# Optimization experiments

Measured on AMD Instinct MI355X. Metric: run time of the kernel, lower is better.

Reference implementation:

```python
import jax, jax.numpy as jnp
import numpy as np

B, C, H, W = 16, 64, 128, 128
C8 = C // 8

def setup_inputs() -> dict:
    key = jax.random.key(0)
    ks = jax.random.split(key, 9)
    s = 0.05
    return {
        "x": jax.random.normal(ks[0], (B, C, H, W), jnp.float32),
        "y": jax.random.normal(ks[1], (B, C, H, W), jnp.float32),
        "query_w": jax.random.normal(ks[2], (C8, C), jnp.float32) * s,
        "query_b": jax.random.normal(ks[3], (C8,), jnp.float32) * s,
        "key_w": jax.random.normal(ks[4], (C8, C), jnp.float32) * s,
        "key_b": jax.random.normal(ks[5], (C8,), jnp.float32) * s,
        "value_w": jax.random.normal(ks[6], (C, 2 * C), jnp.float32) * s,
        "value_b": jax.random.normal(ks[7], (C,), jnp.float32) * s,
        "gamma": jax.random.normal(ks[8], (), jnp.float32) * 0.1,
    }

def _conv1x1(t, w, b):
    # t: [B, Cin, H, W], w: [Cout, Cin] -> [B, Cout, H, W]
    return jnp.einsum('oc,bchw->bohw', w, t) + b[None, :, None, None]

def reference(x, y, query_w, query_b, key_w, key_b, value_w, value_b, gamma):
    b, c, h, w = x.shape
    q = _conv1x1(x, query_w, query_b)                       # [B, C8, H, W]
    k = _conv1x1(y, key_w, key_b)                           # [B, C8, H, W]
    v = _conv1x1(jnp.concatenate([x, y], axis=1), value_w, value_b)  # [B, C, H, W]

    # axial energies: H-axis (g indexes key rows), W-axis (u indexes key cols)
    energy_H = jnp.einsum('bchw,bcgw->bhwg', q, k)          # [B, H, W, H]
    energy_W = jnp.einsum('bchw,bchu->bhwu', q, k)          # [B, H, W, W]

    # -inf on the H diagonal (self position counted once, via the W branch)
    eye = jnp.eye(h, dtype=bool)                            # [H, H]
    energy_H = jnp.where(eye[None, :, None, :], -jnp.inf, energy_H)

    att = jax.nn.softmax(jnp.concatenate([energy_H, energy_W], axis=3), axis=3)
    att_H = att[..., :h]                                    # [B, H, W, H]
    att_W = att[..., h:]                                    # [B, H, W, W]

    out_H = jnp.einsum('bcgw,bhwg->bchw', v, att_H)
    out_W = jnp.einsum('bchu,bhwu->bchw', v, att_W)
    return gamma * (out_H + out_W) + x + y
```

## Files before the change

kernel.cpp:

```cpp
#include <hip/hip_runtime.h>

#define NCH 80
#define HW 16384

typedef unsigned short u16;
typedef unsigned int u32;
typedef short s16x8 __attribute__((ext_vector_type(8)));
typedef float f32x4 __attribute__((ext_vector_type(4)));

__device__ __forceinline__ float b2f_lo(u32 pk){ union{u32 u; float f;} c; c.u = pk<<16; return c.f; }
__device__ __forceinline__ float b2f_hi(u32 pk){ union{u32 u; float f;} c; c.u = pk & 0xffff0000u; return c.f; }
__device__ __forceinline__ float b2f(u16 v){ union{u32 u; float f;} c; c.u = ((u32)v)<<16; return c.f; }
__device__ __forceinline__ u16 f2b_hw(float f){
    union{ __bf16 h; u16 s; } c; c.h = (__bf16)f; return c.s;
}
__device__ __forceinline__ u32 pk2(float a, float b){
    return (u32)f2b_hw(a) | ((u32)f2b_hw(b)<<16);
}
#define NEG_INF (-__builtin_inff())

__global__ __launch_bounds__(256) void k_wcvt(
    const float* __restrict__ qw, const float* __restrict__ qb,
    const float* __restrict__ kw, const float* __restrict__ kb,
    const float* __restrict__ vw, const float* __restrict__ vb,
    u16* __restrict__ wbf, float* __restrict__ bias80)
{
    int i = blockIdx.x*256 + threadIdx.x;
    int ch = i >> 7, cin = i & 127;
    float v;
    if (ch < 8)       v = (cin < 64) ? qw[ch*64 + cin] : 0.f;
    else if (ch < 16) v = (cin >= 64) ? kw[(ch-8)*64 + (cin-64)] : 0.f;
    else              v = vw[(ch-16)*128 + cin];
    wbf[i] = f2b_hw(v);
    if (i < 80){
        bias80[i] = (i<8) ? qb[i] : (i<16) ? kb[i-8] : vb[i-16];
    }
}

__global__ __launch_bounds__(256) void k_qkv_mfma(
    const float* __restrict__ x, const float* __restrict__ y,
    const u16* __restrict__ wbf, const float* __restrict__ bias80,
    u16* __restrict__ qkv, u16* __restrict__ xy)
{
    int t = threadIdx.x;
    int wv = t >> 6, l = t & 63;
    int lm = l & 15, q = l >> 4;
    int p0 = blockIdx.x * 64 + wv * 16;
    int b = p0 >> 14, rem = p0 & 16383;

    const float* xb = x + (size_t)b*64*HW + rem + lm;
    const float* yb = y + (size_t)b*64*HW + rem + lm;
    float xf[4][8];
    #pragma unroll
    for (int ks=0; ks<4; ks++){
        const float* srcp = (ks < 2) ? xb : yb;
        int cin0 = (ks & 1)*32 + q*8;
        #pragma unroll
        for (int j=0;j<8;j++) xf[ks][j] = srcp[(size_t)(cin0 + j)*HW];
    }
    s16x8 af[4];
    #pragma unroll
    for (int ks=0; ks<4; ks++)
        #pragma unroll
        for (int j=0;j<8;j++) af[ks][j] = (short)f2b_hw(xf[ks][j]);

    if (xy){
        #pragma unroll
        for (int half=0; half<2; half++)
            #pragma unroll
            for (int j=0;j<8;j++){
                int c = half*32 + q*8 + j;
                xy[(size_t)(b*64+c)*HW + rem + lm] = f2b_hw(xf[half][j] + xf[half+2][j]);
            }
    }

    f32x4 acc[5];
    #pragma unroll
    for (int mt=0; mt<5; mt++) acc[mt] = (f32x4){0.f,0.f,0.f,0.f};

    #pragma unroll
    for (int mt=0; mt<5; mt++){
        int ch = mt*16 + lm;
        const u16* wrow = wbf + ch*128 + q*8;
        #pragma unroll
        for (int ks=0; ks<4; ks++){
            s16x8 bfrag = *(const s16x8*)(wrow + ks*32);
            acc[mt] = __builtin_amdgcn_mfma_f32_16x16x32_bf16(af[ks], bfrag, acc[mt], 0, 0, 0);
        }
    }

    #pragma unroll
    for (int mt=0; mt<5; mt++){
        int ch = mt*16 + lm;
        float bs = bias80[ch];
        u32 lo = pk2(acc[mt][0]+bs, acc[mt][1]+bs);
        u32 hi = pk2(acc[mt][2]+bs, acc[mt][3]+bs);
        *(uint2*)&qkv[(size_t)(b*NCH + ch)*HW + rem + q*4] = make_uint2(lo, hi);
    }
}

__global__ __launch_bounds__(256) void k_tr(const u16* __restrict__ src, u16* __restrict__ dst)
{
    __shared__ u16 tile[64][65];
    int blk = blockIdx.x;
    int plane = blk >> 2, tq = blk & 3;
    int r0 = (tq >> 1) * 64, c0 = (tq & 1) * 64;
    const u16* s = src + (size_t)plane * HW;
    u16* d = dst + (size_t)plane * HW;
    int col = threadIdx.x & 63, rr = threadIdx.x >> 6;
    #pragma unroll
    for (int k=0;k<16;k++){
        int r = k*4 + rr;
        tile[r][col] = s[(r0+r)*128 + c0 + col];
    }
    __syncthreads();
    #pragma unroll
    for (int k=0;k<16;k++){
        int r = k*4 + rr;
        d[(c0+r)*128 + r0 + col] = tile[col][r];
    }
}

__global__ __launch_bounds__(512, 4) void k_col(
    const u16* __restrict__ qkvT, u16* __restrict__ colT,
    float* __restrict__ mH, float* __restrict__ sH)
{
    __shared__ __align__(16) float q_s[8*128];
    __shared__ __align__(16) float k_sw[8*128];
    __shared__ __align__(16) u16  v_bf[64*128];
    __shared__ __align__(16) u16  p_bf[128*128];

    int t = threadIdx.x;
    int b = blockIdx.x >> 7, w = blockIdx.x & 127;
    const u32* src = (const u32*)(qkvT + (size_t)b*NCH*HW + w*128);
    u32* v32 = (u32*)v_bf;
    u32* p32 = (u32*)p_bf;

    #pragma unroll
    for (int r=0;r<2;r++){
        int idx = t + r*512;
        int ch = idx >> 6, hp = idx & 63;
        u32 pk = src[ch*8192 + hp];
        int g0 = hp*2;
        if (ch < 8){
            *(float2*)&q_s[ch*128 + g0] = make_float2(b2f_lo(pk), b2f_hi(pk));
        } else {
            int o = ch - 8;
            k_sw[g0*8     + (o ^ ((g0>>3)&7))]     = b2f_lo(pk);
            k_sw[(g0+1)*8 + (o ^ (((g0+1)>>3)&7))] = b2f_hi(pk);
        }
    }
    #pragma unroll
    for (int r=0;r<8;r++){
        int idx = t + r*512;
        int c = idx >> 6, gp = idx & 63;
        v32[(c*64 + gp) ^ ((c&7)<<2)] = src[(16+c)*8192 + gp];
    }
    __syncthreads();

    int tr = t >> 4, tc = t & 15;
    int h0 = tr*4, g0 = tc*8;
    float e[4][8];
    #pragma unroll
    for (int i=0;i<4;i++)
        #pragma unroll
        for (int j=0;j<8;j++) e[i][j] = 0.f;

    #pragma unroll
    for (int o=0;o<8;o++){
        float qv[4], kv[8];
        #pragma unroll
        for (int i=0;i<4;i++) qv[i] = q_s[o*128 + h0 + i];
        int kb = o ^ (tc & 7);
        #pragma unroll
        for (int j=0;j<8;j++) kv[j] = k_sw[(g0+j)*8 + kb];
        #pragma unroll
        for (int i=0;i<4;i++)
            #pragma unroll
            for (int j=0;j<8;j++) e[i][j] += qv[i]*kv[j];
    }
    #pragma unroll
    for (int i=0;i<4;i++){
        int h = h0 + i;
        if ((h>>3) == tc) e[i][h&7] = NEG_INF;
    }
    #pragma unroll
    for (int i=0;i<4;i++){
        int h = h0 + i;
        float m = e[i][0];
        #pragma unroll
        for (int j=1;j<8;j++) m = fmaxf(m, e[i][j]);
        m = fmaxf(m, __shfl_xor(m,1));
        m = fmaxf(m, __shfl_xor(m,2));
        m = fmaxf(m, __shfl_xor(m,4));
        m = fmaxf(m, __shfl_xor(m,8));
        float s = 0.f;
        #pragma unroll
        for (int j=0;j<8;j++){ float pp = __expf(e[i][j]-m); e[i][j]=pp; s += pp; }
        s += __shfl_xor(s,1);
        s += __shfl_xor(s,2);
        s += __shfl_xor(s,4);
        s += __shfl_xor(s,8);
        if (tc == 0){
            mH[b*HW + h*128 + w] = m;
            sH[b*HW + h*128 + w] = s;
        }
        uint4 pw;
        pw.x = pk2(e[i][0], e[i][1]);
        pw.y = pk2(e[i][2], e[i][3]);
        pw.z = pk2(e[i][4], e[i][5]);
        pw.w = pk2(e[i][6], e[i][7]);
        *(uint4*)&p32[(h*64 + tc*4) ^ ((h&7)<<2)] = pw;
    }
    __syncthreads();

    int wv = t >> 6, l = t & 63;
    int lm = l & 15, lq = l >> 4;
    int mt = wv;
    f32x4 acc[4];
    #pragma unroll
    for (int nt=0; nt<4; nt++) acc[nt] = (f32x4){0.f,0.f,0.f,0.f};

    #pragma unroll
    for (int ks=0; ks<4; ks++){
        int ri = mt*16 + lm;
        s16x8 a = *(const s16x8*)&p32[(ri*64 + ks*16 + lq*4) ^ ((ri&7)<<2)];
        #pragma unroll
        for (int nt=0; nt<4; nt++){
            int c = nt*16 + lm;
            s16x8 bf_ = *(const s16x8*)&v32[(c*64 + ks*16 + lq*4) ^ ((c&7)<<2)];
            acc[nt] = __builtin_amdgcn_mfma_f32_16x16x32_bf16(a, bf_, acc[nt], 0, 0, 0);
        }
    }
    #pragma unroll
    for (int nt=0; nt<4; nt++){
        int c = nt*16 + lm;
        int hh = mt*16 + lq*4;
        uint2 st;
        st.x = pk2(acc[nt][0], acc[nt][1]);
        st.y = pk2(acc[nt][2], acc[nt][3]);
        *(uint2*)&colT[((size_t)(b*64+c)*128 + w)*128 + hh] = st;
    }
}

__global__ __launch_bounds__(512, 4) void k_row(
    const u16* __restrict__ qkv, const u16* __restrict__ colpart,
    const float* __restrict__ mH, const float* __restrict__ sH,
    const float* __restrict__ x, const float* __restrict__ y,
    const u16* __restrict__ xy,
    const float* __restrict__ gamma_p, float* __restrict__ out)
{
    __shared__ __align__(16) float q_s[8*128];
    __shared__ __align__(16) float k_sw[8*128];
    __shared__ __align__(16) u16  v_bf[64*128];
    __shared__ __align__(16) u16  p_bf[128*128];
    __shared__ float fc_s[128], fr_s[128];

    int t = threadIdx.x;
    int b = blockIdx.x >> 7, h = blockIdx.x & 127;
    const u32* src = (const u32*)(qkv + (size_t)b*NCH*HW + h*128);
    u32* v32 = (u32*)v_bf;
    u32* p32 = (u32*)p_bf;

    #pragma unroll
    for (int r=0;r<2;r++){
        int idx = t + r*512;
        int ch = idx >> 6, wp = idx & 63;
        u32 pk = src[ch*8192 + wp];
        int u0 = wp*2;
        if (ch < 8){
            *(float2*)&q_s[ch*128 + u0] = make_float2(b2f_lo(pk), b2f_hi(pk));
        } else {
            int o = ch - 8;
            k_sw[u0*8     + (o ^ ((u0>>3)&7))]     = b2f_lo(pk);
            k_sw[(u0+1)*8 + (o ^ (((u0+1)>>3)&7))] = b2f_hi(pk);
        }
    }
    #pragma unroll
    for (int r=0;r<8;r++){
        int idx = t + r*512;
        int c = idx >> 6, up = idx & 63;
        v32[(c*64 + up) ^ ((c&7)<<2)] = src[(16+c)*8192 + up];
    }
    __syncthreads();

    int tr = t >> 4, tc = t & 15;
    int w0 = tr*4, u0 = tc*8;
    float e[4][8];
    #pragma unroll
    for (int i=0;i<4;i++)
        #pragma unroll
        for (int j=0;j<8;j++) e[i][j] = 0.f;

    #pragma unroll
    for (int o=0;o<8;o++){
        float qv[4], kv[8];
        #pragma unroll
        for (int i=0;i<4;i++) qv[i] = q_s[o*128 + w0 + i];
        int kb = o ^ (tc & 7);
        #pragma unroll
        for (int j=0;j<8;j++) kv[j] = k_sw[(u0+j)*8 + kb];
        #pragma unroll
        for (int i=0;i<4;i++)
            #pragma unroll
            for (int j=0;j<8;j++) e[i][j] += qv[i]*kv[j];
    }
    int pixbase = b*HW + h*128;
    #pragma unroll
    for (int i=0;i<4;i++){
        int wp = w0 + i;
        float m = e[i][0];
        #pragma unroll
        for (int j=1;j<8;j++) m = fmaxf(m, e[i][j]);
        m = fmaxf(m, __shfl_xor(m,1));
        m = fmaxf(m, __shfl_xor(m,2));
        m = fmaxf(m, __shfl_xor(m,4));
        m = fmaxf(m, __shfl_xor(m,8));
        float mh = mH[pixbase + wp];
        float sh = sH[pixbase + wp];
        float mg = fmaxf(m, mh);
        float s = 0.f;
        #pragma unroll
        for (int j=0;j<8;j++){ float pp = __expf(e[i][j]-mg); e[i][j]=pp; s += pp; }
        s += __shfl_xor(s,1);
        s += __shfl_xor(s,2);
        s += __shfl_xor(s,4);
        s += __shfl_xor(s,8);
        if (tc == 0){
            float ef = __expf(mh - mg);
            float stot = sh*ef + s;
            fc_s[wp] = ef/stot;
            fr_s[wp] = 1.0f/stot;
        }
        uint4 pw;
        pw.x = pk2(e[i][0], e[i][1]);
        pw.y = pk2(e[i][2], e[i][3]);
        pw.z = pk2(e[i][4], e[i][5]);
        pw.w = pk2(e[i][6], e[i][7]);
        *(uint4*)&p32[(wp*64 + tc*4) ^ ((wp&7)<<2)] = pw;
    }
    __syncthreads();

    int wv = t >> 6, l = t & 63;
    int lm = l & 15, lq = l >> 4;
    int mt = wv;
    f32x4 acc[4];
    #pragma unroll
    for (int nt=0; nt<4; nt++) acc[nt] = (f32x4){0.f,0.f,0.f,0.f};

    #pragma unroll
    for (int ks=0; ks<4; ks++){
        int ri = mt*16 + lm;
        s16x8 a = *(const s16x8*)&p32[(ri*64 + ks*16 + lq*4) ^ ((ri&7)<<2)];
        #pragma unroll
        for (int nt=0; nt<4; nt++){
            int c = nt*16 + lm;
            s16x8 bf_ = *(const s16x8*)&v32[(c*64 + ks*16 + lq*4) ^ ((c&7)<<2)];
            acc[nt] = __builtin_amdgcn_mfma_f32_16x16x32_bf16(a, bf_, acc[nt], 0, 0, 0);
        }
    }
    float gm = gamma_p[0];
    int wq0 = mt*16 + lq*4;
    float fcv[4], frv[4];
    #pragma unroll
    for (int r2=0;r2<4;r2++){ fcv[r2] = fc_s[wq0+r2]; frv[r2] = fr_s[wq0+r2]; }

    #pragma unroll
    for (int nt=0; nt<4; nt++){
        int c = nt*16 + lm;
        size_t off = ((size_t)(b*64+c)*128 + h)*128 + wq0;
        uint2 cpv = *(const uint2*)&colpart[off];
        float cp[4] = {b2f_lo(cpv.x), b2f_hi(cpv.x), b2f_lo(cpv.y), b2f_hi(cpv.y)};
        float xs[4];
        if (xy){
            uint2 xv = *(const uint2*)&xy[off];
            xs[0]=b2f_lo(xv.x); xs[1]=b2f_hi(xv.x); xs[2]=b2f_lo(xv.y); xs[3]=b2f_hi(xv.y);
        } else {
            float4 x4 = *(const float4*)&x[off];
            float4 y4 = *(const float4*)&y[off];
            xs[0]=x4.x+y4.x; xs[1]=x4.y+y4.y; xs[2]=x4.z+y4.z; xs[3]=x4.w+y4.w;
        }
        float4 o4;
        o4.x = gm*(cp[0]*fcv[0] + acc[nt][0]*frv[0]) + xs[0];
        o4.y = gm*(cp[1]*fcv[1] + acc[nt][1]*frv[1]) + xs[1];
        o4.z = gm*(cp[2]*fcv[2] + acc[nt][2]*frv[2]) + xs[2];
        o4.w = gm*(cp[3]*fcv[3] + acc[nt][3]*frv[3]) + xs[3];
        *(float4*)&out[off] = o4;
    }
}

extern "C" void kernel_launch(void* const* d_in, const int* in_sizes, int n_in,
                              void* d_out, int out_size, void* d_ws, size_t ws_size,
                              hipStream_t stream)
{
    (void)in_sizes; (void)n_in; (void)out_size;
    const float* x  = (const float*)d_in[0];
    const float* y  = (const float*)d_in[1];
    const float* qw = (const float*)d_in[2];
    const float* qb = (const float*)d_in[3];
    const float* kw = (const float*)d_in[4];
    const float* kb = (const float*)d_in[5];
    const float* vw = (const float*)d_in[6];
    const float* vb = (const float*)d_in[7];
    const float* gm = (const float*)d_in[8];
    float* out = (float*)d_out;

    char* ws = (char*)d_ws;
    u16* qkv     = (u16*)(ws);
    u16* qkvT    = (u16*)(ws + 41943040ull);
    u16* colT    = (u16*)(ws + 83886080ull);
    u16* colpart = qkvT;
    float* mH    = (float*)(ws + 117440512ull);
    float* sH    = (float*)(ws + 118489088ull);
    u16* wbf     = (u16*)(ws + 119537664ull);
    float* bias80= (float*)(ws + 119558144ull);
    u16* xybuf   = nullptr;
    if (ws_size >= 119603200ull + 33554432ull)
        xybuf = (u16*)(ws + 119603200ull);

    k_wcvt<<<40, 256, 0, stream>>>(qw, qb, kw, kb, vw, vb, wbf, bias80);
    k_qkv_mfma<<<4096, 256, 0, stream>>>(x, y, wbf, bias80, qkv, xybuf);
    k_tr <<<5120, 256, 0, stream>>>(qkv, qkvT);
    k_col<<<2048, 512, 0, stream>>>(qkvT, colT, mH, sH);
    k_tr <<<4096, 256, 0, stream>>>(colT, colpart);
    k_row<<<2048, 512, 0, stream>>>(qkv, colpart, mH, sH, x, y, xybuf, gm, out);
}
```

Before: 193.5 us.

## Stage QKV projection inputs through LDS with vectorized loads and packed xy writes

The QKV projection kernel now loads x/y with float4 reads into a padded shared-memory tile of bf16 pairs, then builds MFMA A-fragments from LDS. Each block covers 128 pixels instead of 64, so the grid is halved. The xy sum buffer is written as packed u32 pairs instead of scalar u16 stores. This targets the uncoalesced scalar global loads and narrow stores of the old version, at the cost of about 33 KB of LDS per block and a block-wide barrier. The xy sum is now computed from bf16-rounded inputs rather than the fp32 values, which changes numerics slightly.

Result: faster. 180.7 us (-6.6%).

```diff
diff --git a/kernel.cpp b/kernel.cpp
--- a/kernel.cpp
+++ b/kernel.cpp
@@ -18,6 +18,8 @@
     return (u32)f2b_hw(a) | ((u32)f2b_hw(b)<<16);
 }
 #define NEG_INF (-__builtin_inff())
+
+union U4S8 { uint4 u; s16x8 v; };
 
 __global__ __launch_bounds__(256) void k_wcvt(
     const float* __restrict__ qw, const float* __restrict__ qb,
@@ -37,65 +39,83 @@
     }
 }
 
-__global__ __launch_bounds__(256) void k_qkv_mfma(
+__global__ __launch_bounds__(256, 4) void k_qkv_mfma(
     const float* __restrict__ x, const float* __restrict__ y,
     const u16* __restrict__ wbf, const float* __restrict__ bias80,
     u16* __restrict__ qkv, u16* __restrict__ xy)
 {
+    __shared__ u32 a32[128*65];
+
     int t = threadIdx.x;
+    int p0 = blockIdx.x * 128;
+    int b = p0 >> 14, rem = p0 & 16383;
+    const float* xb = x + (size_t)b*64*HW + rem;
+    const float* yb = y + (size_t)b*64*HW + rem;
+
+    #pragma unroll
+    for (int r=0;r<8;r++){
+        int idx = t + r*256;
+        int cp = idx >> 5;
+        int pxg = (idx & 31) * 4;
+        const float* srcp = (cp < 32) ? xb : yb;
+        int c0 = (cp & 31)*2;
+        float4 fa = *(const float4*)&srcp[(size_t)c0*HW + pxg];
+        float4 fb = *(const float4*)&srcp[(size_t)(c0+1)*HW + pxg];
+        a32[(pxg+0)*65 + cp] = pk2(fa.x, fb.x);
+        a32[(pxg+1)*65 + cp] = pk2(fa.y, fb.y);
+        a32[(pxg+2)*65 + cp] = pk2(fa.z, fb.z);
+        a32[(pxg+3)*65 + cp] = pk2(fa.w, fb.w);
+    }
+    __syncthreads();
+
+    if (xy){
+        #pragma unroll
+        for (int r=0;r<16;r++){
+            int idx = t + r*256;
+            int c = idx >> 6;
+            int pxp = idx & 63;
+            int cpx = c >> 1, cpy = 32 + (c >> 1);
+            u32 wx0 = a32[(2*pxp)*65 + cpx], wx1 = a32[(2*pxp+1)*65 + cpx];
+            u32 wy0 = a32[(2*pxp)*65 + cpy], wy1 = a32[(2*pxp+1)*65 + cpy];
+            float xv0 = (c&1)? b2f_hi(wx0) : b2f_lo(wx0);
+            float xv1 = (c&1)? b2f_hi(wx1) : b2f_lo(wx1);
+            float yv0 = (c&1)? b2f_hi(wy0) : b2f_lo(wy0);
+            float yv1 = (c&1)? b2f_hi(wy1) : b2f_lo(wy1);
+            size_t xw = ((size_t)(b*64+c)*HW + rem) >> 1;
+            ((u32*)xy)[xw + pxp] = pk2(xv0+yv0, xv1+yv1);
+        }
+    }
+
     int wv = t >> 6, l = t & 63;
-    int lm = l & 15, q = l >> 4;
-    int p0 = blockIdx.x * 64 + wv * 16;
-    int b = p0 >> 14, rem = p0 & 16383;
-
-    const float* xb = x + (size_t)b*64*HW + rem + lm;
-    const float* yb = y + (size_t)b*64*HW + rem + lm;
-    float xf[4][8];
-    #pragma unroll
-    for (int ks=0; ks<4; ks++){
-        const float* srcp = (ks < 2) ? xb : yb;
-        int cin0 = (ks & 1)*32 + q*8;
-        #pragma unroll
-        for (int j=0;j<8;j++) xf[ks][j] = srcp[(size_t)(cin0 + j)*HW];
-    }
-    s16x8 af[4];
-    #pragma unroll
-    for (int ks=0; ks<4; ks++)
-        #pragma unroll
-        for (int j=0;j<8;j++) af[ks][j] = (short)f2b_hw(xf[ks][j]);
-
-    if (xy){
-        #pragma unroll
-        for (int half=0; half<2; half++)
+    int lm = l & 15, lq = l >> 4;
+
+    #pragma unroll
+    for (int m2=0;m2<2;m2++){
+        int pxl = (wv*2 + m2)*16 + lm;
+        s16x8 af[4];
+        #pragma unroll
+        for (int ks=0;ks<4;ks++){
+            int wbase = pxl*65 + ks*16 + lq*4;
+            U4S8 uu;
+            uu.u = make_uint4(a32[wbase], a32[wbase+1], a32[wbase+2], a32[wbase+3]);
+            af[ks] = uu.v;
+        }
+        #pragma unroll
+        for (int nt=0;nt<5;nt++){
+            int ch = nt*16 + lm;
+            const u16* wrow = wbf + ch*128 + lq*8;
+            f32x4 acc = (f32x4){0.f,0.f,0.f,0.f};
             #pragma unroll
-            for (int j=0;j<8;j++){
-                int c = half*32 + q*8 + j;
-                xy[(size_t)(b*64+c)*HW + rem + lm] = f2b_hw(xf[half][j] + xf[half+2][j]);
+            for (int ks=0;ks<4;ks++){
+                s16x8 bfrag = *(const s16x8*)(wrow + ks*32);
+                acc = __builtin_amdgcn_mfma_f32_16x16x32_bf16(af[ks], bfrag, acc, 0, 0, 0);
             }
-    }
-
-    f32x4 acc[5];
-    #pragma unroll
-    for (int mt=0; mt<5; mt++) acc[mt] = (f32x4){0.f,0.f,0.f,0.f};
-
-    #pragma unroll
-    for (int mt=0; mt<5; mt++){
-        int ch = mt*16 + lm;
-        const u16* wrow = wbf + ch*128 + q*8;
-        #pragma unroll
-        for (int ks=0; ks<4; ks++){
-            s16x8 bfrag = *(const s16x8*)(wrow + ks*32);
-            acc[mt] = __builtin_amdgcn_mfma_f32_16x16x32_bf16(af[ks], bfrag, acc[mt], 0, 0, 0);
-        }
-    }
-
-    #pragma unroll
-    for (int mt=0; mt<5; mt++){
-        int ch = mt*16 + lm;
-        float bs = bias80[ch];
-        u32 lo = pk2(acc[mt][0]+bs, acc[mt][1]+bs);
-        u32 hi = pk2(acc[mt][2]+bs, acc[mt][3]+bs);
-        *(uint2*)&qkv[(size_t)(b*NCH + ch)*HW + rem + q*4] = make_uint2(lo, hi);
+            float bs = bias80[ch];
+            int pxs = (wv*2+m2)*16 + lq*4;
+            u32 lo = pk2(acc[0]+bs, acc[1]+bs);
+            u32 hi = pk2(acc[2]+bs, acc[3]+bs);
+            *(uint2*)&qkv[(size_t)(b*NCH + ch)*HW + rem + pxs] = make_uint2(lo, hi);
+        }
     }
 }
 
@@ -419,7 +439,7 @@
         xybuf = (u16*)(ws + 119603200ull);
 
     k_wcvt<<<40, 256, 0, stream>>>(qw, qb, kw, kb, vw, vb, wbf, bias80);
-    k_qkv_mfma<<<4096, 256, 0, stream>>>(x, y, wbf, bias80, qkv, xybuf);
+    k_qkv_mfma<<<2048, 256, 0, stream>>>(x, y, wbf, bias80, qkv, xybuf);
     k_tr <<<5120, 256, 0, stream>>>(qkv, qkvT);
     k_col<<<2048, 512, 0, stream>>>(qkvT, colT, mH, sH);
     k_tr <<<4096, 256, 0, stream>>>(colT, colpart);
```
